# Kernel optimization log

Hardware: AMD Instinct MI355X
Metric: run time of the kernel (lower is better)

## Reference

```python
import jax, jax.numpy as jnp
import numpy as np

N_NODES = 100000
N_EDGES = 1600000
NODE_IN = 64
EDGE_DIM = 32
NODE_OUT = 64


def setup_inputs() -> dict:
    key = jax.random.key(0)
    ks = jax.random.split(key, 8)
    return {
        "nfeats": jax.random.normal(ks[0], (N_NODES, NODE_IN), dtype=jnp.float32),
        "efeats": jax.random.normal(ks[1], (N_EDGES, EDGE_DIM), dtype=jnp.float32),
        "src": jax.random.randint(ks[2], (N_EDGES,), 0, N_NODES, dtype=jnp.int32),
        "dst": jax.random.randint(ks[3], (N_EDGES,), 0, N_NODES, dtype=jnp.int32),
        "W_msg_w": jax.random.normal(ks[4], (NODE_IN + EDGE_DIM, NODE_OUT), dtype=jnp.float32) * 0.1,
        "W_msg_b": jax.random.normal(ks[5], (NODE_OUT,), dtype=jnp.float32) * 0.1,
        "W_apply_w": jax.random.normal(ks[6], (NODE_IN + NODE_OUT, NODE_OUT), dtype=jnp.float32) * 0.1,
        "W_apply_b": jax.random.normal(ks[7], (NODE_OUT,), dtype=jnp.float32) * 0.1,
    }


def reference(nfeats, efeats, src, dst, W_msg_w, W_msg_b, W_apply_w, W_apply_b):
    n_nodes = nfeats.shape[0]
    # message: gather source node features, concat edge features, linear
    m = jnp.concatenate([nfeats[src], efeats], axis=-1) @ W_msg_w + W_msg_b  # [E, node_out]
    # per-destination mean (DGL fn.mean); zero for isolated nodes
    s = jax.ops.segment_sum(m, dst, num_segments=n_nodes)                     # [N, node_out]
    cnt = jax.ops.segment_sum(jnp.ones((m.shape[0],), m.dtype), dst, num_segments=n_nodes)
    h_neigh = s / jnp.maximum(cnt, 1.0)[:, None]
    # apply: concat self features with aggregated messages, linear, activation
    h = jnp.concatenate([nfeats, h_neigh], axis=-1) @ W_apply_w + W_apply_b   # [N, node_out]
    return jax.nn.relu(h)
```

## Files before the change

kernel.cpp:

```cpp
#include <hip/hip_runtime.h>

#define NN 100000
#define NE 1600000
#define NBIN 782
#define CAP  3072
#define EPB  8192
#define NBLKE 196

#define OFF_BINSZ   100004
#define OFF_BINBASE 100788
#define OFF_MASK    101572
#define OFF_EINFO   300520
#define OFF_G       3500520
#define OFF_HM      OFF_G
#define OFF_OM      (OFF_G + 153272)
#define OFF_WCOMB   13100520
#define OFF_BMW     13110760

__global__ __launch_bounds__(256) void k_bhist(const int4* __restrict__ dst4,
                                               int* __restrict__ hm) {
  __shared__ int h[NBIN];
  int b = blockIdx.x, t = threadIdx.x;
  for (int i = t; i < NBIN; i += 256) h[i] = 0;
  __syncthreads();
  int e0 = b * EPB;
#pragma unroll
  for (int i = 0; i < EPB / 1024; ++i) {
    int f = i * 256 + t;
    int e = e0 + f * 4;
    if (e < NE) {
      int4 d = dst4[(e0 >> 2) + f];
      atomicAdd(&h[d.x >> 7], 1);
      atomicAdd(&h[d.y >> 7], 1);
      atomicAdd(&h[d.z >> 7], 1);
      atomicAdd(&h[d.w >> 7], 1);
    }
  }
  __syncthreads();
  for (int i = t; i < NBIN; i += 256) hm[b * NBIN + i] = h[i];
}

__global__ __launch_bounds__(256) void k_bscan(const int* __restrict__ hm,
                                               int* __restrict__ om,
                                               int* __restrict__ binsz) {
  int w = (blockIdx.x * 256 + threadIdx.x) >> 6;
  int lane = threadIdx.x & 63;
  if (w >= NBIN) return;
  int carry = 0;
  for (int base = 0; base < NBLKE; base += 64) {
    int b = base + lane;
    int v = (b < NBLKE) ? hm[b * NBIN + w] : 0;
    int inc = v;
#pragma unroll
    for (int off = 1; off < 64; off <<= 1) {
      int x = __shfl_up(inc, off);
      if (lane >= off) inc += x;
    }
    if (b < NBLKE) om[b * NBIN + w] = carry + inc - v;
    carry += __shfl(inc, 63);
  }
  if (lane == 0) binsz[w] = carry;
}

__global__ __launch_bounds__(1024) void k_binscan(const int* __restrict__ binsz,
                                                  int* __restrict__ binbase) {
  __shared__ int s[1024];
  int t = threadIdx.x;
  int v = (t < NBIN) ? binsz[t] : 0;
  s[t] = v; __syncthreads();
#pragma unroll
  for (int off = 1; off < 1024; off <<= 1) {
    int x = (t >= off) ? s[t - off] : 0;
    __syncthreads();
    s[t] += x;
    __syncthreads();
  }
  if (t <= NBIN) binbase[t] = s[t] - v;
}

__global__ __launch_bounds__(256) void k_bplace(
    const int4* __restrict__ src4, const int4* __restrict__ dst4,
    const int* __restrict__ om, const int* __restrict__ binbase,
    int2* __restrict__ einfo) {
  __shared__ int2 buf[EPB];
  __shared__ int hstart[1024];
  __shared__ int hcur[1024];
  __shared__ int obase[NBIN];
  __shared__ int tscan[256];
  int b = blockIdx.x, t = threadIdx.x;
  int e0 = b * EPB;
  for (int i = t; i < 1024; i += 256) hcur[i] = 0;
  for (int i = t; i < NBIN; i += 256) obase[i] = binbase[i] + om[b * NBIN + i];
  __syncthreads();
#pragma unroll
  for (int i = 0; i < EPB / 1024; ++i) {
    int f = i * 256 + t;
    int e = e0 + f * 4;
    if (e < NE) {
      int4 d = dst4[(e0 >> 2) + f];
      atomicAdd(&hcur[d.x >> 7], 1);
      atomicAdd(&hcur[d.y >> 7], 1);
      atomicAdd(&hcur[d.z >> 7], 1);
      atomicAdd(&hcur[d.w >> 7], 1);
    }
  }
  __syncthreads();
  int base4 = t * 4;
  int v0 = hcur[base4], v1 = hcur[base4 + 1], v2 = hcur[base4 + 2], v3 = hcur[base4 + 3];
  int s = v0 + v1 + v2 + v3;
  tscan[t] = s;
  __syncthreads();
#pragma unroll
  for (int off = 1; off < 256; off <<= 1) {
    int x = (t >= off) ? tscan[t - off] : 0;
    __syncthreads();
    tscan[t] += x;
    __syncthreads();
  }
  int texcl = tscan[t] - s;
  hstart[base4]     = texcl;
  hstart[base4 + 1] = texcl + v0;
  hstart[base4 + 2] = texcl + v0 + v1;
  hstart[base4 + 3] = texcl + v0 + v1 + v2;
  __syncthreads();
  for (int i = t; i < 1024; i += 256) hcur[i] = hstart[i];
  __syncthreads();
#pragma unroll
  for (int i = 0; i < EPB / 1024; ++i) {
    int f = i * 256 + t;
    int e = e0 + f * 4;
    if (e < NE) {
      int4 d = dst4[(e0 >> 2) + f];
      int4 sv = src4[(e0 >> 2) + f];
      int p0 = atomicAdd(&hcur[d.x >> 7], 1);
      int p1 = atomicAdd(&hcur[d.y >> 7], 1);
      int p2 = atomicAdd(&hcur[d.z >> 7], 1);
      int p3 = atomicAdd(&hcur[d.w >> 7], 1);
      buf[p0] = make_int2(sv.x | ((d.x & 127) << 20), (e)     | ((d.x >> 7) << 21));
      buf[p1] = make_int2(sv.y | ((d.y & 127) << 20), (e + 1) | ((d.y >> 7) << 21));
      buf[p2] = make_int2(sv.z | ((d.z & 127) << 20), (e + 2) | ((d.z >> 7) << 21));
      buf[p3] = make_int2(sv.w | ((d.w & 127) << 20), (e + 3) | ((d.w >> 7) << 21));
    }
  }
  __syncthreads();
  int nE = NE - e0; if (nE > EPB) nE = EPB;
  for (int i = t; i < nE; i += 256) {
    int2 r = buf[i];
    int bin = (unsigned)r.y >> 21;
    int pos = obase[bin] + (i - hstart[bin]);
    einfo[pos] = make_int2(r.x, r.y & 0x1FFFFF);
  }
}

__global__ __launch_bounds__(512, 6) void k_sortgather(
    const float* __restrict__ nf, const float* __restrict__ ef,
    const int2* __restrict__ einfo, const int* __restrict__ binbase,
    float* __restrict__ g, float* __restrict__ mask) {
  __shared__ int2 buf[CAP];
  __shared__ int hist[128];
  __shared__ int excl[128];
  __shared__ int sstart[129];
  int b = blockIdx.x, t = threadIdx.x;
  int base = binbase[b];
  int nE = binbase[b + 1] - base;
  int nS = nE < CAP ? nE : CAP;
  if (t < 128) hist[t] = 0;
  __syncthreads();
  int2 myreg[6];
#pragma unroll
  for (int i = 0; i < 6; ++i) {
    int idx = i * 512 + t;
    if (idx < nS) {
      myreg[i] = einfo[base + idx];
      atomicAdd(&hist[(myreg[i].x >> 20) & 127], 1);
    } else {
      myreg[i] = make_int2(-1, 0);
    }
  }
  __syncthreads();
  int myc = 0;
  if (t < 128) { myc = hist[t]; excl[t] = myc; }
  __syncthreads();
#pragma unroll
  for (int off = 1; off < 128; off <<= 1) {
    int x = 0;
    if (t < 128 && t >= off) x = excl[t - off];
    __syncthreads();
    if (t < 128) excl[t] += x;
    __syncthreads();
  }
  if (t < 128) {
    int node = b * 128 + t;
    if (node < NN) mask[node] = myc ? 1.f : 0.f;
    sstart[t] = excl[t] - myc;
    hist[t] = excl[t] - myc;
    if (t == 127) sstart[128] = excl[127];
  }
  __syncthreads();
#pragma unroll
  for (int i = 0; i < 6; ++i) {
    if (myreg[i].x >= 0) {
      int dl = (myreg[i].x >> 20) & 127;
      int p = atomicAdd(&hist[dl], 1);
      buf[p] = make_int2(myreg[i].x & 0xFFFFF, myreg[i].y);
    }
  }
  __syncthreads();
  int wv = t >> 6, lane = t & 63;
  bool hi = lane >= 32;
  int l32 = lane & 31;
  for (int k = 0; k < 16; ++k) {
    int dl = wv * 16 + k;
    int node = b * 128 + dl;
    if (node >= NN) break;
    int beg = sstart[dl], end = sstart[dl + 1];
    int deg = end - beg;
    float a0 = 0.f, a1 = 0.f;
    int j = beg;
    for (; j + 8 <= end; j += 8) {
      int2 q0 = buf[j + 0];
      int2 q1 = buf[j + 1];
      int2 q2 = buf[j + 2];
      int2 q3 = buf[j + 3];
      int2 q4 = buf[j + 4];
      int2 q5 = buf[j + 5];
      int2 q6 = buf[j + 6];
      int2 q7 = buf[j + 7];
      int ep0 = hi ? q1.y : q0.y;
      int ep1 = hi ? q3.y : q2.y;
      int ep2 = hi ? q5.y : q4.y;
      int ep3 = hi ? q7.y : q6.y;
      float v0 = nf[q0.x * 64 + lane];
      float v1 = nf[q1.x * 64 + lane];
      float v2 = nf[q2.x * 64 + lane];
      float v3 = nf[q3.x * 64 + lane];
      float v4 = nf[q4.x * 64 + lane];
      float v5 = nf[q5.x * 64 + lane];
      float v6 = nf[q6.x * 64 + lane];
      float v7 = nf[q7.x * 64 + lane];
      float w0 = ef[ep0 * 32 + l32];
      float w1 = ef[ep1 * 32 + l32];
      float w2 = ef[ep2 * 32 + l32];
      float w3 = ef[ep3 * 32 + l32];
      a0 += ((v0 + v1) + (v2 + v3)) + ((v4 + v5) + (v6 + v7));
      a1 += (w0 + w1) + (w2 + w3);
    }
    for (; j + 2 <= end; j += 2) {
      int2 q0 = buf[j];
      int2 q1 = buf[j + 1];
      int ep = hi ? q1.y : q0.y;
      float v0 = nf[q0.x * 64 + lane];
      float v1 = nf[q1.x * 64 + lane];
      float w0 = ef[ep * 32 + l32];
      a0 += v0 + v1;
      a1 += w0;
    }
    if (j < end) {
      int2 q0 = buf[j];
      a0 += nf[q0.x * 64 + lane];
      if (!hi) a1 += ef[q0.y * 32 + l32];
    }
    a1 += __shfl_down(a1, 32);
    float inv = deg > 0 ? 1.f / (float)deg : 0.f;
    g[node * 96 + lane] = a0 * inv;
    if (!hi) g[node * 96 + 64 + l32] = a1 * inv;
  }
}

__global__ __launch_bounds__(256) void k_pre1(
    const float* __restrict__ Wm, const float* __restrict__ bm,
    const float* __restrict__ Wa, float* __restrict__ Wcomb,
    float* __restrict__ bmW) {
  int b = blockIdx.x, t = threadIdx.x;
  if (b < 24) {
    int o = b * 256 + t;
    int k = o >> 6, j = o & 63;
    float acc = 0.f;
    for (int kk = 0; kk < 64; ++kk)
      acc += Wm[k * 64 + kk] * Wa[(64 + kk) * 64 + j];
    Wcomb[(64 + k) * 64 + j] = acc;
  } else {
    for (int i = t; i < 64 * 64; i += 256) Wcomb[i] = Wa[i];
    if (t < 64) {
      float acc = 0.f;
      for (int kk = 0; kk < 64; ++kk) acc += bm[kk] * Wa[(64 + kk) * 64 + t];
      bmW[t] = acc;
    }
  }
}

__global__ __launch_bounds__(256) void k_main(
    const float4* __restrict__ nf4, const float4* __restrict__ g4,
    const float* __restrict__ mask,
    const float4* __restrict__ Wcomb4, const float* __restrict__ bmW,
    const float* __restrict__ ba, float* __restrict__ out) {
  __shared__ float sA[128 * 33];
  __shared__ float sB[32 * 64];
  int tid = threadIdx.x;
  int ty = tid >> 3, tx = tid & 7;
  int nbase = blockIdx.x * 128;
  float acc[4][8];
#pragma unroll
  for (int r = 0; r < 4; ++r)
#pragma unroll
    for (int e = 0; e < 8; ++e) acc[r][e] = 0.f;

  for (int c = 0; c < 5; ++c) {
#pragma unroll
    for (int i = 0; i < 4; ++i) {
      int f = i * 256 + tid;
      int nl = f >> 3, q = f & 7;
      int node = nbase + nl; if (node > NN - 1) node = NN - 1;
      float4 v;
      if (c < 2) {
        v = nf4[node * 16 + c * 8 + q];
      } else {
        v = g4[node * 24 + (c - 2) * 8 + q];
      }
      float* p = &sA[nl * 33 + q * 4];
      p[0] = v.x; p[1] = v.y; p[2] = v.z; p[3] = v.w;
    }
#pragma unroll
    for (int i = 0; i < 2; ++i) {
      int f = i * 256 + tid;
      int kk = f >> 4, j4 = f & 15;
      float4 w = Wcomb4[(c * 32 + kk) * 16 + j4];
      *(float4*)&sB[kk * 64 + j4 * 4] = w;
    }
    __syncthreads();
#pragma unroll 8
    for (int kk = 0; kk < 32; ++kk) {
      float4 b0 = *(const float4*)&sB[kk * 64 + tx * 8];
      float4 b1 = *(const float4*)&sB[kk * 64 + tx * 8 + 4];
#pragma unroll
      for (int r = 0; r < 4; ++r) {
        float a = sA[(ty * 4 + r) * 33 + kk];
        acc[r][0] += a * b0.x; acc[r][1] += a * b0.y;
        acc[r][2] += a * b0.z; acc[r][3] += a * b0.w;
        acc[r][4] += a * b1.x; acc[r][5] += a * b1.y;
        acc[r][6] += a * b1.z; acc[r][7] += a * b1.w;
      }
    }
    __syncthreads();
  }
  float4 ba0 = ((const float4*)ba)[tx * 2];
  float4 ba1 = ((const float4*)ba)[tx * 2 + 1];
  float4 bw0 = ((const float4*)bmW)[tx * 2];
  float4 bw1 = ((const float4*)bmW)[tx * 2 + 1];
#pragma unroll
  for (int r = 0; r < 4; ++r) {
    int node = nbase + ty * 4 + r;
    if (node < NN) {
      float mk = mask[node];
      float4 o0, o1;
      o0.x = acc[r][0] + ba0.x + mk * bw0.x;
      o0.y = acc[r][1] + ba0.y + mk * bw0.y;
      o0.z = acc[r][2] + ba0.z + mk * bw0.z;
      o0.w = acc[r][3] + ba0.w + mk * bw0.w;
      o1.x = acc[r][4] + ba1.x + mk * bw1.x;
      o1.y = acc[r][5] + ba1.y + mk * bw1.y;
      o1.z = acc[r][6] + ba1.z + mk * bw1.z;
      o1.w = acc[r][7] + ba1.w + mk * bw1.w;
      o0.x = fmaxf(o0.x, 0.f); o0.y = fmaxf(o0.y, 0.f);
      o0.z = fmaxf(o0.z, 0.f); o0.w = fmaxf(o0.w, 0.f);
      o1.x = fmaxf(o1.x, 0.f); o1.y = fmaxf(o1.y, 0.f);
      o1.z = fmaxf(o1.z, 0.f); o1.w = fmaxf(o1.w, 0.f);
      *(float4*)&out[node * 64 + tx * 8] = o0;
      *(float4*)&out[node * 64 + tx * 8 + 4] = o1;
    }
  }
}

extern "C" void kernel_launch(void* const* d_in, const int* in_sizes, int n_in,
                              void* d_out, int out_size, void* d_ws, size_t ws_size,
                              hipStream_t stream) {
  const float* nf = (const float*)d_in[0];
  const float* ef = (const float*)d_in[1];
  const int*   src = (const int*)d_in[2];
  const int*   dst = (const int*)d_in[3];
  const float* Wm = (const float*)d_in[4];
  const float* bm = (const float*)d_in[5];
  const float* Wa = (const float*)d_in[6];
  const float* ba = (const float*)d_in[7];
  int*   wsi = (int*)d_ws;
  float* wsf = (float*)d_ws;
  int*   binsz   = wsi + OFF_BINSZ;
  int*   binbase = wsi + OFF_BINBASE;
  int2*  einfo   = (int2*)(wsi + OFF_EINFO);
  int*   hm      = wsi + OFF_HM;
  int*   om      = wsi + OFF_OM;
  float* mask    = wsf + OFF_MASK;
  float* g       = wsf + OFF_G;
  float* Wcomb   = wsf + OFF_WCOMB;
  float* bmW     = wsf + OFF_BMW;
  float* out = (float*)d_out;

  k_pre1<<<25, 256, 0, stream>>>(Wm, bm, Wa, Wcomb, bmW);
  k_bhist<<<NBLKE, 256, 0, stream>>>((const int4*)dst, hm);
  k_bscan<<<(NBIN * 64 + 255) / 256, 256, 0, stream>>>(hm, om, binsz);
  k_binscan<<<1, 1024, 0, stream>>>(binsz, binbase);
  k_bplace<<<NBLKE, 256, 0, stream>>>((const int4*)src, (const int4*)dst, om,
                                      binbase, einfo);
  k_sortgather<<<NBIN, 512, 0, stream>>>(nf, ef, einfo, binbase, g, mask);
  k_main<<<(NN + 127) / 128, 256, 0, stream>>>(
      (const float4*)nf, (const float4*)g, mask,
      (const float4*)Wcomb, bmW, ba, out);
}
```

Baseline: 184.5 us.

## Gather source node features as bf16 packed pairs in sort-gather kernel

Adds a pre-pass that converts node features to packed bf16 pairs, staged in the output buffer, and has the gather kernel read 128-byte rows instead of 256-byte rows. Each half-wave now handles a different edge, so one wave processes two edges per load and the unroll grows to 16 edges. The halves are combined with a cross-lane shuffle before the mean is written. This cuts random-gather traffic for node features but rounds them to bf16 before aggregation, adding precision error, plus an extra conversion pass over the feature matrix.

```diff
diff --git a/kernel.cpp b/kernel.cpp
--- a/kernel.cpp
+++ b/kernel.cpp
@@ -1,4 +1,5 @@
 #include <hip/hip_runtime.h>
+#include <hip/hip_bf16.h>
 
 #define NN 100000
 #define NE 1600000
@@ -16,6 +17,22 @@
 #define OFF_OM      (OFF_G + 153272)
 #define OFF_WCOMB   13100520
 #define OFF_BMW     13110760
+
+__global__ __launch_bounds__(256) void k_cvt(const float4* __restrict__ nf4,
+                                             uint4* __restrict__ nfb) {
+  int t = blockIdx.x * 256 + threadIdx.x;
+  float4 a = nf4[t * 2], b = nf4[t * 2 + 1];
+  uint4 o;
+  o.x = ((uint)__bfloat16_as_ushort(__float2bfloat16(a.x))) |
+        ((uint)__bfloat16_as_ushort(__float2bfloat16(a.y)) << 16);
+  o.y = ((uint)__bfloat16_as_ushort(__float2bfloat16(a.z))) |
+        ((uint)__bfloat16_as_ushort(__float2bfloat16(a.w)) << 16);
+  o.z = ((uint)__bfloat16_as_ushort(__float2bfloat16(b.x))) |
+        ((uint)__bfloat16_as_ushort(__float2bfloat16(b.y)) << 16);
+  o.w = ((uint)__bfloat16_as_ushort(__float2bfloat16(b.z))) |
+        ((uint)__bfloat16_as_ushort(__float2bfloat16(b.w)) << 16);
+  nfb[t] = o;
+}
 
 __global__ __launch_bounds__(256) void k_bhist(const int4* __restrict__ dst4,
                                                int* __restrict__ hm) {
@@ -153,7 +170,7 @@
 }
 
 __global__ __launch_bounds__(512, 6) void k_sortgather(
-    const float* __restrict__ nf, const float* __restrict__ ef,
+    const uint* __restrict__ nfb, const float* __restrict__ ef,
     const int2* __restrict__ einfo, const int* __restrict__ binbase,
     float* __restrict__ g, float* __restrict__ mask) {
   __shared__ int2 buf[CAP];
@@ -215,9 +232,9 @@
     if (node >= NN) break;
     int beg = sstart[dl], end = sstart[dl + 1];
     int deg = end - beg;
-    float a0 = 0.f, a1 = 0.f;
+    float a0x = 0.f, a0y = 0.f, a1 = 0.f;
     int j = beg;
-    for (; j + 8 <= end; j += 8) {
+    for (; j + 16 <= end; j += 16) {
       int2 q0 = buf[j + 0];
       int2 q1 = buf[j + 1];
       int2 q2 = buf[j + 2];
@@ -226,44 +243,84 @@
       int2 q5 = buf[j + 5];
       int2 q6 = buf[j + 6];
       int2 q7 = buf[j + 7];
-      int ep0 = hi ? q1.y : q0.y;
-      int ep1 = hi ? q3.y : q2.y;
-      int ep2 = hi ? q5.y : q4.y;
-      int ep3 = hi ? q7.y : q6.y;
-      float v0 = nf[q0.x * 64 + lane];
-      float v1 = nf[q1.x * 64 + lane];
-      float v2 = nf[q2.x * 64 + lane];
-      float v3 = nf[q3.x * 64 + lane];
-      float v4 = nf[q4.x * 64 + lane];
-      float v5 = nf[q5.x * 64 + lane];
-      float v6 = nf[q6.x * 64 + lane];
-      float v7 = nf[q7.x * 64 + lane];
-      float w0 = ef[ep0 * 32 + l32];
-      float w1 = ef[ep1 * 32 + l32];
-      float w2 = ef[ep2 * 32 + l32];
-      float w3 = ef[ep3 * 32 + l32];
-      a0 += ((v0 + v1) + (v2 + v3)) + ((v4 + v5) + (v6 + v7));
-      a1 += (w0 + w1) + (w2 + w3);
+      int2 q8 = buf[j + 8];
+      int2 q9 = buf[j + 9];
+      int2 qa = buf[j + 10];
+      int2 qb = buf[j + 11];
+      int2 qc = buf[j + 12];
+      int2 qd = buf[j + 13];
+      int2 qe = buf[j + 14];
+      int2 qf = buf[j + 15];
+      int n0 = hi ? q1.x : q0.x;
+      int n1 = hi ? q3.x : q2.x;
+      int n2 = hi ? q5.x : q4.x;
+      int n3 = hi ? q7.x : q6.x;
+      int n4 = hi ? q9.x : q8.x;
+      int n5 = hi ? qb.x : qa.x;
+      int n6 = hi ? qd.x : qc.x;
+      int n7 = hi ? qf.x : qe.x;
+      int e0 = hi ? q1.y : q0.y;
+      int e1 = hi ? q3.y : q2.y;
+      int e2 = hi ? q5.y : q4.y;
+      int e3 = hi ? q7.y : q6.y;
+      int e4 = hi ? q9.y : q8.y;
+      int e5 = hi ? qb.y : qa.y;
+      int e6 = hi ? qd.y : qc.y;
+      int e7 = hi ? qf.y : qe.y;
+      uint u0 = nfb[n0 * 32 + l32];
+      uint u1 = nfb[n1 * 32 + l32];
+      uint u2 = nfb[n2 * 32 + l32];
+      uint u3 = nfb[n3 * 32 + l32];
+      uint u4 = nfb[n4 * 32 + l32];
+      uint u5 = nfb[n5 * 32 + l32];
+      uint u6 = nfb[n6 * 32 + l32];
+      uint u7 = nfb[n7 * 32 + l32];
+      float w0 = ef[e0 * 32 + l32];
+      float w1 = ef[e1 * 32 + l32];
+      float w2 = ef[e2 * 32 + l32];
+      float w3 = ef[e3 * 32 + l32];
+      float w4 = ef[e4 * 32 + l32];
+      float w5 = ef[e5 * 32 + l32];
+      float w6 = ef[e6 * 32 + l32];
+      float w7 = ef[e7 * 32 + l32];
+      a0x += __uint_as_float(u0 << 16) + __uint_as_float(u1 << 16)
+           + __uint_as_float(u2 << 16) + __uint_as_float(u3 << 16)
+           + __uint_as_float(u4 << 16) + __uint_as_float(u5 << 16)
+           + __uint_as_float(u6 << 16) + __uint_as_float(u7 << 16);
+      a0y += __uint_as_float(u0 & 0xFFFF0000u) + __uint_as_float(u1 & 0xFFFF0000u)
+           + __uint_as_float(u2 & 0xFFFF0000u) + __uint_as_float(u3 & 0xFFFF0000u)
+           + __uint_as_float(u4 & 0xFFFF0000u) + __uint_as_float(u5 & 0xFFFF0000u)
+           + __uint_as_float(u6 & 0xFFFF0000u) + __uint_as_float(u7 & 0xFFFF0000u);
+      a1 += ((w0 + w1) + (w2 + w3)) + ((w4 + w5) + (w6 + w7));
     }
     for (; j + 2 <= end; j += 2) {
       int2 q0 = buf[j];
       int2 q1 = buf[j + 1];
-      int ep = hi ? q1.y : q0.y;
-      float v0 = nf[q0.x * 64 + lane];
-      float v1 = nf[q1.x * 64 + lane];
-      float w0 = ef[ep * 32 + l32];
-      a0 += v0 + v1;
+      int n0 = hi ? q1.x : q0.x;
+      int e0 = hi ? q1.y : q0.y;
+      uint u0 = nfb[n0 * 32 + l32];
+      float w0 = ef[e0 * 32 + l32];
+      a0x += __uint_as_float(u0 << 16);
+      a0y += __uint_as_float(u0 & 0xFFFF0000u);
       a1 += w0;
     }
     if (j < end) {
       int2 q0 = buf[j];
-      a0 += nf[q0.x * 64 + lane];
-      if (!hi) a1 += ef[q0.y * 32 + l32];
-    }
+      if (!hi) {
+        uint u0 = nfb[q0.x * 32 + l32];
+        a0x += __uint_as_float(u0 << 16);
+        a0y += __uint_as_float(u0 & 0xFFFF0000u);
+        a1 += ef[q0.y * 32 + l32];
+      }
+    }
+    a0x += __shfl_xor(a0x, 32);
+    a0y += __shfl_xor(a0y, 32);
     a1 += __shfl_down(a1, 32);
     float inv = deg > 0 ? 1.f / (float)deg : 0.f;
-    g[node * 96 + lane] = a0 * inv;
-    if (!hi) g[node * 96 + 64 + l32] = a1 * inv;
+    if (!hi) {
+      *(float2*)&g[node * 96 + l32 * 2] = make_float2(a0x * inv, a0y * inv);
+      g[node * 96 + 64 + l32] = a1 * inv;
+    }
   }
 }
 
@@ -394,14 +451,16 @@
   float* Wcomb   = wsf + OFF_WCOMB;
   float* bmW     = wsf + OFF_BMW;
   float* out = (float*)d_out;
-
+  uint*  nfb = (uint*)d_out;
+
+  k_cvt<<<NN * 64 / 8 / 256, 256, 0, stream>>>((const float4*)nf, (uint4*)nfb);
   k_pre1<<<25, 256, 0, stream>>>(Wm, bm, Wa, Wcomb, bmW);
   k_bhist<<<NBLKE, 256, 0, stream>>>((const int4*)dst, hm);
   k_bscan<<<(NBIN * 64 + 255) / 256, 256, 0, stream>>>(hm, om, binsz);
   k_binscan<<<1, 1024, 0, stream>>>(binsz, binbase);
   k_bplace<<<NBLKE, 256, 0, stream>>>((const int4*)src, (const int4*)dst, om,
                                       binbase, einfo);
-  k_sortgather<<<NBIN, 512, 0, stream>>>(nf, ef, einfo, binbase, g, mask);
+  k_sortgather<<<NBIN, 512, 0, stream>>>(nfb, ef, einfo, binbase, g, mask);
   k_main<<<(NN + 127) / 128, 256, 0, stream>>>(
       (const float4*)nf, (const float4*)g, mask,
       (const float4*)Wcomb, bmW, ba, out);
```

New measurement: 162.8 us. 11.8% less time.
